# Kernel tuning notes

Hardware: AMD Instinct MI355X
Metric: run time of the kernel (lower is better)

Reference implementation:

```python
import jax, jax.numpy as jnp
import numpy as np

B, N, DX, DZ = 4, 2048, 2, 128
PPD = (128, 128)
GRID_RANGE = ((-2.0, 2.0), (-2.0, 2.0))
INIT_LS = 0.1


def _construct_grid():
    axes = [jnp.linspace(lo, hi, p, dtype=jnp.float32) for (lo, hi), p in zip(GRID_RANGE, PPD)]
    mesh = jnp.meshgrid(*axes, indexing="ij")
    return jnp.stack(mesh, axis=-1)  # [128, 128, 2]


def setup_inputs() -> dict:
    key = jax.random.key(0)
    k1, k2 = jax.random.split(key)
    x = jax.random.uniform(k1, (B, N, DX), dtype=jnp.float32, minval=-2.0, maxval=2.0)
    z = jax.random.normal(k2, (B, N, DZ), dtype=jnp.float32)
    grid = _construct_grid()
    # inverse-softplus of init lengthscale, per dim
    ls0 = jnp.full((DX,), INIT_LS, dtype=jnp.float32)
    lengthscale_param = jnp.log(jnp.exp(ls0) - 1.0)
    return {"x": x, "z": z, "grid": grid, "lengthscale_param": lengthscale_param}


def reference(x, z, grid, lengthscale_param):
    b = x.shape[0]
    grid_shape = grid.shape[:-1]  # (128, 128)
    lengthscale = 1e-05 + jax.nn.softplus(lengthscale_param)  # [dx]
    grid_flat = grid.reshape(-1, grid.shape[-1])  # [M, dx], M = 16384
    # per-dim squared distance / l^2, summed over dx  -> [b, M, n]
    diff = grid_flat[None, :, None, :] - x[:, None, :, :]  # [b, M, n, dx]
    pre_exp = jnp.sum((diff * diff) / (lengthscale ** 2), axis=-1)
    weights = jnp.exp(-0.5 * pre_exp)  # [b, M, n]
    z_grid_flat = jnp.einsum("bmn,bnd->bmd", weights, z)  # [b, M, dz]
    z_grid = z_grid_flat.reshape((b,) + grid_shape + (z.shape[-1],))
    x_grid = jnp.broadcast_to(grid[None], (b,) + grid.shape)
    return (x_grid, z_grid)
```

## Files before the change

### kernel.cpp

```cpp
#include <hip/hip_runtime.h>

#define BATCH 4
#define NPTS  2048
#define DZDIM 128
#define GD    128
#define M_TOT (GD*GD)
#define TN    32
#define PW    40
#define PZ    40
#define ZP    2112
#define WBIN  15

typedef __attribute__((ext_vector_type(8))) __bf16 bf16x8;
typedef __attribute__((ext_vector_type(4))) float floatx4;

__device__ __forceinline__ unsigned int f2bf_bits(float x){
  unsigned int u = __float_as_uint(x);
  u += 0x7FFFu + ((u >> 16) & 1u);
  return u >> 16;
}
__device__ __forceinline__ int point_bin(float px){
  int bin = __float2int_rn((px + 2.0f) * (127.0f / 4.0f));
  return min(GD - 1, max(0, bin));
}

__global__ __launch_bounds__(256) void hist_xgrid_kernel(
    const float* __restrict__ x, const float* __restrict__ grid,
    float* __restrict__ out, int* __restrict__ binStart)
{
  const int tid = threadIdx.x;
  if (blockIdx.x < BATCH){
    __shared__ int h[GD];
    __shared__ int s[GD + 1];
    const int b = blockIdx.x;
    if (tid < GD) h[tid] = 0;
    __syncthreads();
    for (int n = tid; n < NPTS; n += 256)
      atomicAdd(&h[point_bin(x[(b*NPTS + n)*2])], 1);
    __syncthreads();
    if (tid == 0){
      int acc = 0;
#pragma unroll
      for (int j = 0; j < GD; ++j){ s[j] = acc; acc += h[j]; }
      s[GD] = acc;
    }
    __syncthreads();
    if (tid <= GD) binStart[b*(GD+1) + tid] = s[tid];
  } else {
    int idx = (blockIdx.x - BATCH) * 256 + tid;
    float g = grid[idx];
#pragma unroll
    for (int b = 0; b < BATCH; ++b) out[b*(GD*GD*2) + idx] = g;
  }
}

__global__ __launch_bounds__(256) void scatter_kernel(const float* __restrict__ x,
                                                      const int* __restrict__ binStart,
                                                      float2* __restrict__ xs,
                                                      int* __restrict__ perm){
  const int b = blockIdx.y;
  const int wv = threadIdx.x >> 6, lane = threadIdx.x & 63;
  const int bin = blockIdx.x * 4 + wv;
  int base = binStart[b*(GD+1) + bin];
  const float2* __restrict__ x2 = (const float2*)x;
  for (int n0 = 0; n0 < NPTS; n0 += 64){
    int n = n0 + lane;
    float2 xv = x2[b*NPTS + n];
    bool keep = (point_bin(xv.x) == bin);
    unsigned long long mask = __ballot(keep);
    int pre = __popcll(mask & ((1ull << lane) - 1ull));
    if (keep){
      xs[(long)b*ZP + base + pre] = xv;
      perm[b*NPTS + base + pre]   = n;
    }
    base += __popcll(mask);
  }
}

__global__ __launch_bounds__(256) void ztbuild_kernel(const float* __restrict__ z,
                                                      const int* __restrict__ perm,
                                                      unsigned short* __restrict__ zt){
  const int b  = blockIdx.y;
  const int j0 = blockIdx.x * 64;
  const int jj = threadIdx.x & 63;
  const int dq = threadIdx.x >> 6;
  const int j  = j0 + jj;
  const int n  = perm[b*NPTS + j];
  const float4* __restrict__ z4 = (const float4*)z;
  const long rb = (long)(b*NPTS + n) * 32;
#pragma unroll
  for (int r = 0; r < 8; ++r){
    int c = dq*8 + r;
    float4 v = z4[rb + c];
    long o = ((long)(b*DZDIM + 4*c) * ZP) + j;
    zt[o         ] = (unsigned short)f2bf_bits(v.x);
    zt[o +   ZP  ] = (unsigned short)f2bf_bits(v.y);
    zt[o + 2*ZP  ] = (unsigned short)f2bf_bits(v.z);
    zt[o + 3*ZP  ] = (unsigned short)f2bf_bits(v.w);
  }
}

__global__ __launch_bounds__(256, 4) void setconv_mfma_kernel(
    const float2* __restrict__ xs, const int* __restrict__ binStart,
    const unsigned short* __restrict__ zt, const float* __restrict__ lsp,
    float* __restrict__ outz)
{
  __shared__ __align__(16) unsigned short Wlds[2][64 * PW];
  __shared__ __align__(16) unsigned short Zlds[2][DZDIM * PZ];

  const int tid = threadIdx.x, lane = tid & 63, wv = tid >> 6;
  const int bid = blockIdx.x;
  const int g   = bid & 7;
  const int s   = bid >> 3;
  const int h   = s & 1;
  const int b   = (s >> 1) & 3;
  const int il  = s >> 3;
  const int i   = g*16 + il;
  const int my0 = h * 64;

  const float l0 = 1e-5f + log1pf(expf(lsp[0]));
  const float l1 = 1e-5f + log1pf(expf(lsp[1]));
  const float LOG2E = 1.4426950408889634f;
  const float c0 = -0.5f * LOG2E / (l0*l0);
  const float c1 = -0.5f * LOG2E / (l1*l1);
  const float step = 4.0f / 127.0f;
  const float gx   = -2.0f + (float)i * step;

  const int lo  = binStart[b*(GD+1) + max(0, i - WBIN)];
  const int hi  = binStart[b*(GD+1) + min(GD-1, i + WBIN) + 1];
  const int lo8 = lo & ~7;
  const int len = hi - lo8;
  const int T   = (len + TN - 1) / TN;

  const int   wnp = tid & 15;
  const int   mb  = tid >> 4;
  const float gy0 = -2.0f + (float)(my0 + mb) * step;

  int goff[3];
#pragma unroll
  for (int u = 0; u < 3; ++u){
    int gi = wv + 4*u;
    if (gi < 10){
      int pos = gi*64 + lane;
      int d = pos / 5, c = pos % 5;
      if (c > 3) c = 3;
      goff[u] = (b*DZDIM + d) * ZP + c*8;
    } else goff[u] = 0;
  }

  const int q  = lane >> 4;
  const int ml = lane & 15;

  floatx4 acc[8];
#pragma unroll
  for (int tz = 0; tz < 8; ++tz) acc[tz] = (floatx4){0.f, 0.f, 0.f, 0.f};

  auto stageZ = [&](int buf, int t){
    const int k0 = lo8 + t*TN;
#pragma unroll
    for (int u = 0; u < 3; ++u){
      int gi = wv + 4*u;
      if (gi < 10){
        const unsigned short* gp = zt + goff[u] + k0;
        __builtin_amdgcn_global_load_lds(
            (__attribute__((address_space(1))) void*)gp,
            (__attribute__((address_space(3))) void*)&Zlds[buf][gi*512],
            16, 0, 0);
      }
    }
  };
  auto stageW = [&](int buf, int t){
    const int ka = t*TN + 2*wnp;
    float4 xv = *(const float4*)&xs[(long)b*ZP + lo8 + ka];
    float d0a = gx - xv.x, d0b = gx - xv.z;
    float t0a = (ka     < len) ? c0*d0a*d0a : -1.0e30f;
    float t0b = (ka + 1 < len) ? c0*d0b*d0b : -1.0e30f;
#pragma unroll
    for (int r = 0; r < 4; ++r){
      float gy  = gy0 + (float)(16*r) * step;
      float dya = gy - xv.y, dyb = gy - xv.w;
      float ua = fmaf(c1*dya, dya, t0a);
      float ub = fmaf(c1*dyb, dyb, t0b);
      unsigned int v = f2bf_bits(__builtin_amdgcn_exp2f(ua))
                     | (f2bf_bits(__builtin_amdgcn_exp2f(ub)) << 16);
      *(unsigned int*)&Wlds[buf][(mb + 16*r)*PW + 2*wnp] = v;
    }
  };
  auto domfma = [&](int buf){
    bf16x8 af = *(const bf16x8*)&Wlds[buf][(wv*16 + ml)*PW + q*8];
#pragma unroll
    for (int tz = 0; tz < 8; ++tz){
      bf16x8 bf = *(const bf16x8*)&Zlds[buf][(tz*16 + ml)*PZ + q*8];
      acc[tz] = __builtin_amdgcn_mfma_f32_16x16x32_bf16(af, bf, acc[tz], 0, 0, 0);
    }
  };

  if (T > 0){
    stageZ(0, 0);
    stageW(0, 0);
    __syncthreads();
    for (int t = 0; t < T; ++t){
      const int cur = t & 1, nxt = 1 - cur;
      if (t + 1 < T) stageZ(nxt, t + 1);
      domfma(cur);
      if (t + 1 < T) stageW(nxt, t + 1);
      __syncthreads();
    }
  }

  const long obase = ((long)(b*M_TOT + i*GD + my0 + wv*16 + q*4) << 7) + ml;
#pragma unroll
  for (int tz = 0; tz < 8; ++tz)
#pragma unroll
    for (int r = 0; r < 4; ++r)
      outz[obase + ((long)r << 7) + tz*16] = acc[tz][r];
}

extern "C" void kernel_launch(void* const* d_in, const int* in_sizes, int n_in,
                              void* d_out, int out_size, void* d_ws, size_t ws_size,
                              hipStream_t stream)
{
  const float* x    = (const float*)d_in[0];
  const float* z    = (const float*)d_in[1];
  const float* grid = (const float*)d_in[2];
  const float* lsp  = (const float*)d_in[3];
  float* out = (float*)d_out;

  char* ws = (char*)d_ws;
  int*            binStart = (int*)ws;
  int*            perm     = (int*)(ws + 2064);
  float2*         xs       = (float2*)(ws + 2064 + 32768);
  unsigned short* zt       = (unsigned short*)(ws + 2064 + 32768 + 67584);

  hipLaunchKernelGGL(hist_xgrid_kernel, dim3(BATCH + GD), dim3(256), 0, stream,
                     x, grid, out, binStart);
  hipLaunchKernelGGL(scatter_kernel, dim3(GD/4, BATCH), dim3(256), 0, stream,
                     x, binStart, xs, perm);
  hipLaunchKernelGGL(ztbuild_kernel, dim3(NPTS/64, BATCH), dim3(256), 0, stream, z, perm, zt);
  hipLaunchKernelGGL(setconv_mfma_kernel, dim3(GD*2*BATCH), dim3(256), 0, stream,
                     xs, binStart, zt, lsp, out + BATCH*GD*GD*2);
}
```

Before: 110.5 us.

## Drop LDS staging; compute weights per lane and load Z directly to registers

The main kernel no longer stages weights and Z tiles through shared memory with block barriers. Each lane now computes its own bf16 weight fragment in registers and loads its Z B-operand straight from global memory, double-buffered in registers, which removes __syncthreads and LDS traffic. Tile starts are aligned to 32 instead of being masked by length. Padding rows of xs and zt are zeroed in the prep kernel so out-of-range points contribute nothing, and ztbuild uses twice as many blocks. The trade-off is more register pressure, redundant global loads and weight computations across waves, and reliance on the zero padding for correctness.

```diff
diff --git a/kernel.cpp b/kernel.cpp
--- a/kernel.cpp
+++ b/kernel.cpp
@@ -6,13 +6,12 @@
 #define GD    128
 #define M_TOT (GD*GD)
 #define TN    32
-#define PW    40
-#define PZ    40
 #define ZP    2112
 #define WBIN  15
 
 typedef __attribute__((ext_vector_type(8))) __bf16 bf16x8;
 typedef __attribute__((ext_vector_type(4))) float floatx4;
+typedef __attribute__((ext_vector_type(4))) unsigned int uintx4;
 
 __device__ __forceinline__ unsigned int f2bf_bits(float x){
   unsigned int u = __float_as_uint(x);
@@ -24,15 +23,17 @@
   return min(GD - 1, max(0, bin));
 }
 
-__global__ __launch_bounds__(256) void hist_xgrid_kernel(
+__global__ __launch_bounds__(256) void prep_kernel(
     const float* __restrict__ x, const float* __restrict__ grid,
-    float* __restrict__ out, int* __restrict__ binStart)
+    float* __restrict__ out, int* __restrict__ binStart,
+    float2* __restrict__ xs, unsigned short* __restrict__ zt)
 {
   const int tid = threadIdx.x;
-  if (blockIdx.x < BATCH){
+  const int bx  = blockIdx.x;
+  if (bx < BATCH){
     __shared__ int h[GD];
     __shared__ int s[GD + 1];
-    const int b = blockIdx.x;
+    const int b = bx;
     if (tid < GD) h[tid] = 0;
     __syncthreads();
     for (int n = tid; n < NPTS; n += 256)
@@ -46,11 +47,20 @@
     }
     __syncthreads();
     if (tid <= GD) binStart[b*(GD+1) + tid] = s[tid];
+  } else if (bx < BATCH + 128){
+    int idx = (bx - BATCH) * 256 + tid;
+    float g = grid[idx];
+#pragma unroll
+    for (int b = 0; b < BATCH; ++b) out[b*(GD*GD*2) + idx] = g;
+  } else if (bx == BATCH + 128){
+    int b = tid >> 6, j = tid & 63;
+    xs[(size_t)b*ZP + NPTS + j] = make_float2(0.f, 0.f);
   } else {
-    int idx = (blockIdx.x - BATCH) * 256 + tid;
-    float g = grid[idx];
-#pragma unroll
-    for (int b = 0; b < BATCH; ++b) out[b*(GD*GD*2) + idx] = g;
+    int row = (bx - (BATCH + 129)) * 256 + tid;
+    uintx4 zv = {0u, 0u, 0u, 0u};
+    uintx4* p = (uintx4*)&zt[(size_t)row*ZP + NPTS];
+#pragma unroll
+    for (int c = 0; c < 8; ++c) p[c] = zv;
   }
 }
 
@@ -80,7 +90,8 @@
 __global__ __launch_bounds__(256) void ztbuild_kernel(const float* __restrict__ z,
                                                       const int* __restrict__ perm,
                                                       unsigned short* __restrict__ zt){
-  const int b  = blockIdx.y;
+  const int by = blockIdx.y;
+  const int b = by >> 1, half = by & 1;
   const int j0 = blockIdx.x * 64;
   const int jj = threadIdx.x & 63;
   const int dq = threadIdx.x >> 6;
@@ -89,14 +100,14 @@
   const float4* __restrict__ z4 = (const float4*)z;
   const long rb = (long)(b*NPTS + n) * 32;
 #pragma unroll
-  for (int r = 0; r < 8; ++r){
-    int c = dq*8 + r;
+  for (int r = 0; r < 4; ++r){
+    int c = half*16 + dq*4 + r;
     float4 v = z4[rb + c];
     long o = ((long)(b*DZDIM + 4*c) * ZP) + j;
-    zt[o         ] = (unsigned short)f2bf_bits(v.x);
-    zt[o +   ZP  ] = (unsigned short)f2bf_bits(v.y);
-    zt[o + 2*ZP  ] = (unsigned short)f2bf_bits(v.z);
-    zt[o + 3*ZP  ] = (unsigned short)f2bf_bits(v.w);
+    zt[o        ] = (unsigned short)f2bf_bits(v.x);
+    zt[o +   ZP ] = (unsigned short)f2bf_bits(v.y);
+    zt[o + 2*ZP ] = (unsigned short)f2bf_bits(v.z);
+    zt[o + 3*ZP ] = (unsigned short)f2bf_bits(v.w);
   }
 }
 
@@ -105,9 +116,6 @@
     const unsigned short* __restrict__ zt, const float* __restrict__ lsp,
     float* __restrict__ outz)
 {
-  __shared__ __align__(16) unsigned short Wlds[2][64 * PW];
-  __shared__ __align__(16) unsigned short Zlds[2][DZDIM * PZ];
-
   const int tid = threadIdx.x, lane = tid & 63, wv = tid >> 6;
   const int bid = blockIdx.x;
   const int g   = bid & 7;
@@ -126,94 +134,76 @@
   const float step = 4.0f / 127.0f;
   const float gx   = -2.0f + (float)i * step;
 
-  const int lo  = binStart[b*(GD+1) + max(0, i - WBIN)];
-  const int hi  = binStart[b*(GD+1) + min(GD-1, i + WBIN) + 1];
-  const int lo8 = lo & ~7;
-  const int len = hi - lo8;
-  const int T   = (len + TN - 1) / TN;
-
-  const int   wnp = tid & 15;
-  const int   mb  = tid >> 4;
-  const float gy0 = -2.0f + (float)(my0 + mb) * step;
-
-  int goff[3];
-#pragma unroll
-  for (int u = 0; u < 3; ++u){
-    int gi = wv + 4*u;
-    if (gi < 10){
-      int pos = gi*64 + lane;
-      int d = pos / 5, c = pos % 5;
-      if (c > 3) c = 3;
-      goff[u] = (b*DZDIM + d) * ZP + c*8;
-    } else goff[u] = 0;
-  }
-
-  const int q  = lane >> 4;
-  const int ml = lane & 15;
+  const int lo   = binStart[b*(GD+1) + max(0, i - WBIN)];
+  const int hi   = binStart[b*(GD+1) + min(GD-1, i + WBIN) + 1];
+  const int lo32 = lo & ~31;
+  const int T    = (hi - lo32 + TN - 1) / TN;
+
+  const int q  = lane >> 4, ml = lane & 15;
+  const int m  = my0 + wv*16 + ml;
+  const float gym = -2.0f + (float)m * step;
+
+  const unsigned short* __restrict__ ztb = zt + ((size_t)b*DZDIM + ml)*ZP;
+  const float4* __restrict__ xsb = (const float4*)(xs + (size_t)b*ZP);
 
   floatx4 acc[8];
 #pragma unroll
   for (int tz = 0; tz < 8; ++tz) acc[tz] = (floatx4){0.f, 0.f, 0.f, 0.f};
 
-  auto stageZ = [&](int buf, int t){
-    const int k0 = lo8 + t*TN;
-#pragma unroll
-    for (int u = 0; u < 3; ++u){
-      int gi = wv + 4*u;
-      if (gi < 10){
-        const unsigned short* gp = zt + goff[u] + k0;
-        __builtin_amdgcn_global_load_lds(
-            (__attribute__((address_space(1))) void*)gp,
-            (__attribute__((address_space(3))) void*)&Zlds[buf][gi*512],
-            16, 0, 0);
-      }
-    }
+  bf16x8 Ba[8], Bb[8];
+
+  auto loadB = [&](bf16x8* dst, int t){
+    const int k = lo32 + t*TN + q*8;
+#pragma unroll
+    for (int tz = 0; tz < 8; ++tz)
+      dst[tz] = *(const bf16x8*)&ztb[(size_t)(tz*16)*ZP + k];
   };
-  auto stageW = [&](int buf, int t){
-    const int ka = t*TN + 2*wnp;
-    float4 xv = *(const float4*)&xs[(long)b*ZP + lo8 + ka];
-    float d0a = gx - xv.x, d0b = gx - xv.z;
-    float t0a = (ka     < len) ? c0*d0a*d0a : -1.0e30f;
-    float t0b = (ka + 1 < len) ? c0*d0b*d0b : -1.0e30f;
-#pragma unroll
-    for (int r = 0; r < 4; ++r){
-      float gy  = gy0 + (float)(16*r) * step;
-      float dya = gy - xv.y, dyb = gy - xv.w;
-      float ua = fmaf(c1*dya, dya, t0a);
-      float ub = fmaf(c1*dyb, dyb, t0b);
-      unsigned int v = f2bf_bits(__builtin_amdgcn_exp2f(ua))
-                     | (f2bf_bits(__builtin_amdgcn_exp2f(ub)) << 16);
-      *(unsigned int*)&Wlds[buf][(mb + 16*r)*PW + 2*wnp] = v;
-    }
+  auto stepT = [&](const bf16x8* curB, int t){
+    const int kp = lo32 + t*TN + q*8;
+    float4 P0 = xsb[(kp >> 1)    ];
+    float4 P1 = xsb[(kp >> 1) + 1];
+    float4 P2 = xsb[(kp >> 1) + 2];
+    float4 P3 = xsb[(kp >> 1) + 3];
+    float px[8] = {P0.x,P0.z,P1.x,P1.z,P2.x,P2.z,P3.x,P3.z};
+    float py[8] = {P0.y,P0.w,P1.y,P1.w,P2.y,P2.w,P3.y,P3.w};
+    unsigned int u[4];
+#pragma unroll
+    for (int p = 0; p < 4; ++p){
+      float dx0 = gx - px[2*p],   t00 = (c0*dx0)*dx0;
+      float dy0 = gym - py[2*p];
+      float w0  = __builtin_amdgcn_exp2f(fmaf(c1*dy0, dy0, t00));
+      float dx1 = gx - px[2*p+1], t01 = (c0*dx1)*dx1;
+      float dy1 = gym - py[2*p+1];
+      float w1  = __builtin_amdgcn_exp2f(fmaf(c1*dy1, dy1, t01));
+      u[p] = f2bf_bits(w0) | (f2bf_bits(w1) << 16);
+    }
+    union { uintx4 u4; bf16x8 v; } cvt;
+    cvt.u4 = (uintx4){u[0], u[1], u[2], u[3]};
+    bf16x8 af = cvt.v;
+#pragma unroll
+    for (int tz = 0; tz < 8; ++tz)
+      acc[tz] = __builtin_amdgcn_mfma_f32_16x16x32_bf16(af, curB[tz], acc[tz], 0, 0, 0);
   };
-  auto domfma = [&](int buf){
-    bf16x8 af = *(const bf16x8*)&Wlds[buf][(wv*16 + ml)*PW + q*8];
-#pragma unroll
-    for (int tz = 0; tz < 8; ++tz){
-      bf16x8 bf = *(const bf16x8*)&Zlds[buf][(tz*16 + ml)*PZ + q*8];
-      acc[tz] = __builtin_amdgcn_mfma_f32_16x16x32_bf16(af, bf, acc[tz], 0, 0, 0);
-    }
-  };
 
   if (T > 0){
-    stageZ(0, 0);
-    stageW(0, 0);
-    __syncthreads();
-    for (int t = 0; t < T; ++t){
-      const int cur = t & 1, nxt = 1 - cur;
-      if (t + 1 < T) stageZ(nxt, t + 1);
-      domfma(cur);
-      if (t + 1 < T) stageW(nxt, t + 1);
-      __syncthreads();
-    }
-  }
-
-  const long obase = ((long)(b*M_TOT + i*GD + my0 + wv*16 + q*4) << 7) + ml;
+    loadB(Ba, 0);
+    int t = 0;
+    while (true){
+      if (t + 1 < T) loadB(Bb, t + 1);
+      stepT(Ba, t);
+      ++t; if (t >= T) break;
+      if (t + 1 < T) loadB(Ba, t + 1);
+      stepT(Bb, t);
+      ++t; if (t >= T) break;
+    }
+  }
+
+  const size_t obase = ((size_t)(b*M_TOT + i*GD + my0 + wv*16 + q*4) << 7) + ml;
 #pragma unroll
   for (int tz = 0; tz < 8; ++tz)
 #pragma unroll
     for (int r = 0; r < 4; ++r)
-      outz[obase + ((long)r << 7) + tz*16] = acc[tz][r];
+      outz[obase + ((size_t)r << 7) + tz*16] = acc[tz][r];
 }
 
 extern "C" void kernel_launch(void* const* d_in, const int* in_sizes, int n_in,
@@ -232,11 +222,12 @@
   float2*         xs       = (float2*)(ws + 2064 + 32768);
   unsigned short* zt       = (unsigned short*)(ws + 2064 + 32768 + 67584);
 
-  hipLaunchKernelGGL(hist_xgrid_kernel, dim3(BATCH + GD), dim3(256), 0, stream,
-                     x, grid, out, binStart);
+  hipLaunchKernelGGL(prep_kernel, dim3(BATCH + 128 + 3), dim3(256), 0, stream,
+                     x, grid, out, binStart, xs, zt);
   hipLaunchKernelGGL(scatter_kernel, dim3(GD/4, BATCH), dim3(256), 0, stream,
                      x, binStart, xs, perm);
-  hipLaunchKernelGGL(ztbuild_kernel, dim3(NPTS/64, BATCH), dim3(256), 0, stream, z, perm, zt);
+  hipLaunchKernelGGL(ztbuild_kernel, dim3(NPTS/64, BATCH*2), dim3(256), 0, stream,
+                     z, perm, zt);
   hipLaunchKernelGGL(setconv_mfma_kernel, dim3(GD*2*BATCH), dim3(256), 0, stream,
                      xs, binStart, zt, lsp, out + BATCH*GD*GD*2);
 }
```

Measured after the change: 204.7 us. 1.85x slower.
